# Optimization experiments

Hardware: AMD Instinct MI355X
Metric: run time of the kernel (lower is better)

Reference implementation:

```python
import jax, jax.numpy as jnp
import numpy as np

CH = 256
IC = 128  # inter_channels = channels // reduction
TEMP = 0.05


def setup_inputs() -> dict:
    key = jax.random.key(0)
    k1, k2, k3, k4, k5 = jax.random.split(key, 5)
    x = jax.random.normal(k1, (8, CH, 64, 64), dtype=jnp.float32)
    # 1x1 conv weights stored as [out_ch, in_ch]
    w_qkv = jax.random.normal(k2, (3 * IC, CH), dtype=jnp.float32) * 0.01
    b_qkv = jax.random.normal(k3, (3 * IC,), dtype=jnp.float32) * 0.01
    w_out = jax.random.normal(k4, (CH, IC), dtype=jnp.float32) * 0.01
    b_out = jax.random.normal(k5, (CH,), dtype=jnp.float32) * 0.01
    return {"x": x, "w_qkv": w_qkv, "b_qkv": b_qkv, "w_out": w_out, "b_out": b_out}


def reference(x, w_qkv, b_qkv, w_out, b_out):
    b, c, h, w = x.shape
    n = h * w
    ic = w_qkv.shape[0] // 3
    # 1x1 conv QKV projection
    qkv = jnp.einsum('bchw,oc->bohw', x, w_qkv) + b_qkv[None, :, None, None]
    qkv = qkv.reshape(b, 3, ic, n)
    q, k, v = qkv[:, 0], qkv[:, 1], qkv[:, 2]  # each [b, ic, n]
    # mean-center q and k over spatial positions (per channel)
    k = k - k.mean(axis=-1, keepdims=True)
    q = q - q.mean(axis=-1, keepdims=True)
    # pairwise_weight[b, i, j] = sum_c k[b, c, i] * q[b, c, j]
    pw = jnp.einsum('bci,bcj->bij', k, q)
    pw = pw / jnp.sqrt(jnp.float32(ic))  # use_scale=True
    pw = pw / TEMP
    pw = jax.nn.softmax(pw, axis=-1)  # [b, n, n]
    # y[b, c, i] = sum_j pw[b, i, j] * v[b, c, j]
    y = jnp.einsum('bij,bcj->bci', pw, v).reshape(b, ic, h, w)
    out = x + jnp.einsum('bchw,oc->bohw', y, w_out) + b_out[None, :, None, None]
    return out
```

## Files before the change

kernel.cpp:

```cpp
#include <hip/hip_runtime.h>
#include <hip/hip_bf16.h>

typedef __bf16 bf16_t;
typedef __bf16 bf16x8 __attribute__((ext_vector_type(8)));
typedef float f32x4 __attribute__((ext_vector_type(4)));
typedef float f32x16 __attribute__((ext_vector_type(16)));

#define MFMA16(a, b, c) __builtin_amdgcn_mfma_f32_16x16x32_bf16((a), (b), (c), 0, 0, 0)
#define MFMA32(a, b, c) __builtin_amdgcn_mfma_f32_32x32x16_bf16((a), (b), (c), 0, 0, 0)

constexpr int CH = 256, IC = 128, NPOS = 4096;
constexpr float SM_C = 2.5503488f;

constexpr size_t OFF_XT    = 0;
constexpr size_t OFF_QT    = 16777216;
constexpr size_t OFF_KT    = 25165824;
constexpr size_t OFF_V     = 33554432;
constexpr size_t OFF_WQKV  = 41943040;
constexpr size_t OFF_WOUT  = 42139648;
constexpr size_t OFF_QKM   = 42213376;
constexpr size_t OFF_PL    = 42221568;

__device__ __forceinline__ void gload_lds16(const char* g, char* lds) {
    __builtin_amdgcn_global_load_lds((const __attribute__((address_space(1))) unsigned int*)g,
                                     (__attribute__((address_space(3))) unsigned int*)lds, 16, 0,
                                     0);
}
__device__ __forceinline__ float fexp2(float x) {
    float r;
    asm("v_exp_f32 %0, %1" : "=v"(r) : "v"(x));
    return r;
}
__device__ __forceinline__ int cvtpk(float lo, float hi) {
    int r;
    asm("v_cvt_pk_bf16_f32 %0, %1, %2" : "=v"(r) : "v"(lo), "v"(hi));
    return r;
}

__global__ void k_prep1(const float* __restrict__ x, const float* __restrict__ wqkv,
                        const float* __restrict__ wout, bf16_t* __restrict__ xt,
                        float* __restrict__ xpart, bf16_t* __restrict__ wqkv_b,
                        bf16_t* __restrict__ wout_b) {
    int bid = blockIdx.x;
    if (bid >= 8192) {
        int idx = (bid - 8192) * 256 + threadIdx.x;
        if (idx < 384 * 256) wqkv_b[idx] = (bf16_t)wqkv[idx];
        int j = idx - 384 * 256;
        if (j >= 0 && j < 256 * 128) wout_b[j] = (bf16_t)wout[j];
        return;
    }
    __shared__ float t[32][33];
    int p0 = (bid & 127) * 32, c0 = ((bid >> 7) & 7) * 32, b = bid >> 10;
    int i = threadIdx.x >> 5, j = threadIdx.x & 31;
#pragma unroll
    for (int q = 0; q < 4; q++) {
        int c = c0 + q * 8 + i;
        t[q * 8 + i][j] = x[((size_t)(b * CH + c)) * NPOS + p0 + j];
    }
    __syncthreads();
#pragma unroll
    for (int q = 0; q < 4; q++) {
        int p = p0 + q * 8 + i;
        xt[((size_t)(b * NPOS + p)) * CH + c0 + j] = (bf16_t)t[j][q * 8 + i];
    }
    int cl = threadIdx.x >> 3, part = threadIdx.x & 7;
    float s = 0.f;
#pragma unroll
    for (int u = 0; u < 4; u++) s += t[cl][part * 4 + u];
    s += __shfl_down(s, 4, 64);
    s += __shfl_down(s, 2, 64);
    s += __shfl_down(s, 1, 64);
    if (part == 0) xpart[((size_t)(b * 128) + (p0 >> 5)) * 256 + c0 + cl] = s;
}

__global__ void k_small(const float* __restrict__ xpart, const float* __restrict__ wqkv,
                        float* __restrict__ qkm) {
    int b = blockIdx.x, t = threadIdx.x;
    __shared__ float xm[256];
    float s = 0.f;
    const float* xp = xpart + (size_t)(b * 128) * 256 + t;
#pragma unroll 8
    for (int i = 0; i < 128; i++) s += xp[i * 256];
    xm[t] = s * (1.0f / NPOS);
    __syncthreads();
    float acc = 0.f;
    const float4* w = (const float4*)(wqkv + (size_t)t * CH);
#pragma unroll
    for (int c4 = 0; c4 < 64; c4++) {
        float4 w4 = w[c4];
        acc += w4.x * xm[c4 * 4] + w4.y * xm[c4 * 4 + 1] + w4.z * xm[c4 * 4 + 2] +
               w4.w * xm[c4 * 4 + 3];
    }
    qkm[b * CH + t] = acc;
}

__global__ __launch_bounds__(256, 2) void k_qkv(const bf16_t* __restrict__ xt,
                                                const bf16_t* __restrict__ wqkv_b,
                                                const float* __restrict__ qkm,
                                                const float* __restrict__ b_qkv,
                                                bf16_t* __restrict__ qt, bf16_t* __restrict__ kt,
                                                bf16_t* __restrict__ v) {
    int bid = blockIdx.x;
    int b = bid & 7;
    int r0 = bid >> 3;
    int sec = r0 % 3;
    int pt = r0 / 3;
    int p0 = pt * 128;
    int wid = threadIdx.x >> 6, lane = threadIdx.x & 63;
    int g = lane >> 4, li = lane & 15;
    int wr = wid >> 1, wc = wid & 1;
    f32x4 acc[4][4] = {};
    if (sec < 2) {
        int ob = sec * 128;
#pragma unroll 1
        for (int kk = 0; kk < 8; kk++) {
            bf16x8 af[4], bfg[4];
#pragma unroll
            for (int fa = 0; fa < 4; fa++) {
                int p = p0 + wr * 64 + fa * 16 + li;
                af[fa] = *(const bf16x8*)(xt + ((size_t)(b * NPOS + p)) * CH + kk * 32 + g * 8);
            }
#pragma unroll
            for (int fb = 0; fb < 4; fb++) {
                int o = ob + wc * 64 + fb * 16 + li;
                bfg[fb] = *(const bf16x8*)(wqkv_b + (size_t)o * CH + kk * 32 + g * 8);
            }
#pragma unroll
            for (int fa = 0; fa < 4; fa++)
#pragma unroll
                for (int fb = 0; fb < 4; fb++) acc[fa][fb] = MFMA16(af[fa], bfg[fb], acc[fa][fb]);
        }
        bf16_t* dst = (sec == 0) ? qt : kt;
        float scale = (sec == 1) ? SM_C : 1.0f;
#pragma unroll
        for (int fb = 0; fb < 4; fb++) {
            int ol = wc * 64 + fb * 16 + li;
            float mean = qkm[b * CH + sec * 128 + ol];
#pragma unroll
            for (int fa = 0; fa < 4; fa++)
#pragma unroll
                for (int r = 0; r < 4; r++) {
                    int p = p0 + wr * 64 + fa * 16 + g * 4 + r;
                    dst[((size_t)(b * NPOS + p)) * IC + ol] =
                        (bf16_t)((acc[fa][fb][r] - mean) * scale);
                }
        }
    } else {
#pragma unroll 1
        for (int kk = 0; kk < 8; kk++) {
            bf16x8 af[4], bfg[4];
#pragma unroll
            for (int fa = 0; fa < 4; fa++) {
                int o = 256 + wr * 64 + fa * 16 + li;
                af[fa] = *(const bf16x8*)(wqkv_b + (size_t)o * CH + kk * 32 + g * 8);
            }
#pragma unroll
            for (int fb = 0; fb < 4; fb++) {
                int p = p0 + wc * 64 + fb * 16 + li;
                bfg[fb] = *(const bf16x8*)(xt + ((size_t)(b * NPOS + p)) * CH + kk * 32 + g * 8);
            }
#pragma unroll
            for (int fa = 0; fa < 4; fa++)
#pragma unroll
                for (int fb = 0; fb < 4; fb++) acc[fa][fb] = MFMA16(af[fa], bfg[fb], acc[fa][fb]);
        }
#pragma unroll
        for (int fa = 0; fa < 4; fa++)
#pragma unroll
            for (int r = 0; r < 4; r++) {
                int oe = wr * 64 + fa * 16 + g * 4 + r;
                float bias = b_qkv[256 + oe];
#pragma unroll
                for (int fb = 0; fb < 4; fb++) {
                    int p = p0 + wc * 64 + fb * 16 + li;
                    v[((size_t)(b * IC + oe)) * NPOS + p] = (bf16_t)(acc[fa][fb][r] + bias);
                }
            }
    }
}

constexpr int TJ = 32;

__global__ __launch_bounds__(256, 2) void k_attn(const bf16_t* __restrict__ qt,
                                                 const bf16_t* __restrict__ kt,
                                                 const bf16_t* __restrict__ v,
                                                 bf16_t* __restrict__ pacc,
                                                 float* __restrict__ pl) {
    __shared__ __attribute__((aligned(128))) char smem[2 * 16384];
    const int bid = blockIdx.x;
    const int b = bid & 7;
    const int jh = (bid >> 3) & 1;
    const int it = bid >> 4;
    const int jbase = jh * 2048;
    const int t = threadIdx.x;
    const int wid = t >> 6, lane = t & 63;
    const int col = lane & 31, h = lane >> 5;
    const int iw0 = it * 128 + wid * 32;
    const bf16_t* ktb = kt + (size_t)b * NPOS * IC;
    const bf16_t* qtb = qt + (size_t)b * NPOS * IC;
    const bf16_t* vb = v + (size_t)b * IC * NPOS;

    int qoff_[2], voff_[2];
#pragma unroll
    for (int u = 0; u < 2; u++) {
        int li2 = u * 256 + t;
        int row = li2 >> 4, p = li2 & 15;
        qoff_[u] = row * 256 + ((p ^ (row & 15)) << 4);
        int g = p ^ (row & 15);
        int c = (g >> 2) * 32 + row;
        voff_[u] = c * 8192 + (g & 3) * 16;
    }

    auto stage = [&](int dstpar, int sj) {
        const char* qs = (const char*)qtb + (size_t)sj * 256;
        const char* vs = (const char*)vb + (size_t)sj * 2;
        char* qd = smem + dstpar * 16384;
        char* vd = qd + 8192;
#pragma unroll
        for (int u = 0; u < 2; u++) {
            gload_lds16(qs + qoff_[u], qd + (u * 256 + t) * 16);
            gload_lds16(vs + voff_[u], vd + (u * 256 + t) * 16);
        }
    };

    bf16x8 bk[8];
#pragma unroll
    for (int ks = 0; ks < 8; ks++)
        bk[ks] = *(const bf16x8*)(ktb + (size_t)(iw0 + col) * IC + ks * 16 + h * 8);

    stage(0, jbase);

    f32x16 acc[4] = {};
    float ls[4] = {0.f, 0.f, 0.f, 0.f};

    auto body = [&](int par, int nextj) {
        stage(par ^ 1, nextj);
        asm volatile("s_waitcnt vmcnt(4)" ::: "memory");
        __builtin_amdgcn_s_barrier();
        asm volatile("" ::: "memory");
        const char* qb = smem + par * 16384;
        const char* vbuf = qb + 8192;
        f32x16 s = {};
        __builtin_amdgcn_s_setprio(1);
#pragma unroll
        for (int ks = 0; ks < 8; ks++) {
            bf16x8 aq = *(const bf16x8*)(qb + col * 256 + (((ks * 2 + h) ^ (col & 15)) << 4));
            s = MFMA32(aq, bk[ks], s);
        }
        __builtin_amdgcn_s_setprio(0);
        float e[16];
#pragma unroll
        for (int r = 0; r < 16; r++) e[r] = fexp2(s[r]);
#pragma unroll
        for (int r = 0; r < 16; r++) ls[r & 3] += e[r];
        int w[8];
#pragma unroll
        for (int q = 0; q < 8; q++) w[q] = cvtpk(e[2 * q], e[2 * q + 1]);
        asm("v_permlane32_swap_b32 %0, %1" : "+v"(w[0]), "+v"(w[2]));
        asm("v_permlane32_swap_b32 %0, %1" : "+v"(w[1]), "+v"(w[3]));
        asm("v_permlane32_swap_b32 %0, %1" : "+v"(w[4]), "+v"(w[6]));
        asm("v_permlane32_swap_b32 %0, %1" : "+v"(w[5]), "+v"(w[7]));
        union {
            int u[4];
            bf16x8 v;
        } pb0, pb1;
        pb0.u[0] = w[0]; pb0.u[1] = w[1]; pb0.u[2] = w[2]; pb0.u[3] = w[3];
        pb1.u[0] = w[4]; pb1.u[1] = w[5]; pb1.u[2] = w[6]; pb1.u[3] = w[7];
        __builtin_amdgcn_s_setprio(1);
#pragma unroll
        for (int kg = 0; kg < 2; kg++) {
            bf16x8 pbf = kg == 0 ? pb0.v : pb1.v;
#pragma unroll
            for (int cs = 0; cs < 4; cs++) {
                bf16x8 av = *(const bf16x8*)(vbuf + col * 256 +
                                             (((cs * 4 + kg * 2 + h) ^ (col & 15)) << 4));
                acc[cs] = MFMA32(av, pbf, acc[cs]);
            }
        }
        __builtin_amdgcn_s_setprio(0);
        asm volatile("" ::: "memory");
        __builtin_amdgcn_s_barrier();
    };

#pragma unroll 1
    for (int jo = 0; jo < 2048; jo += 2 * TJ) {
        body(0, jbase + ((jo + TJ) & 2047));
        body(1, jbase + ((jo + 2 * TJ) & 2047));
    }

    float lsum = (ls[0] + ls[1]) + (ls[2] + ls[3]);
    lsum += __shfl_xor(lsum, 32, 64);
    const int i = iw0 + col;
    if (h == 0) pl[((size_t)(b * 2 + jh)) * NPOS + i] = lsum;

    bf16_t* po = pacc + ((size_t)(b * 2 + jh)) * NPOS * IC;
#pragma unroll
    for (int cs = 0; cs < 4; cs++)
#pragma unroll
        for (int q = 0; q < 8; q++) {
            int u = cvtpk(acc[cs][2 * q], acc[cs][2 * q + 1]);
            int c0 = cs * 32 + ((q & 1) << 1) + ((q >> 1) << 3) + 4 * h;
            *(int*)((char*)po + ((size_t)i * IC + c0) * 2) = u;
        }
}

__global__ __launch_bounds__(256, 2) void k_out(const bf16_t* __restrict__ pacc,
                                                const float* __restrict__ pl,
                                                const bf16_t* __restrict__ wout_b,
                                                const float* __restrict__ x,
                                                const float* __restrict__ b_out,
                                                float* __restrict__ out) {
    int bid = blockIdx.x;
    int b = bid & 7;
    int r0 = bid >> 3;
    int oct = r0 & 1, pt = r0 >> 1;
    int p0 = pt * 128, oc0 = oct * 128;
    int wid = threadIdx.x >> 6, lane = threadIdx.x & 63;
    int g = lane >> 4, li = lane & 15;
    int wr = wid >> 1, wc = wid & 1;
    const bf16_t* pa0 = pacc + (size_t)(b * 2 + 0) * NPOS * IC;
    const bf16_t* pa1 = pacc + (size_t)(b * 2 + 1) * NPOS * IC;
    float inv[4];
#pragma unroll
    for (int fb = 0; fb < 4; fb++) {
        int p = p0 + wc * 64 + fb * 16 + li;
        inv[fb] = 1.0f / (pl[(size_t)(b * 2 + 0) * NPOS + p] + pl[(size_t)(b * 2 + 1) * NPOS + p]);
    }
    f32x4 acc[4][4] = {};
#pragma unroll
    for (int kk = 0; kk < 4; kk++) {
        bf16x8 af[4], bfg[4];
#pragma unroll
        for (int fa = 0; fa < 4; fa++) {
            int oc = oc0 + wr * 64 + fa * 16 + li;
            af[fa] = *(const bf16x8*)(wout_b + (size_t)oc * IC + kk * 32 + g * 8);
        }
#pragma unroll
        for (int fb = 0; fb < 4; fb++) {
            int p = p0 + wc * 64 + fb * 16 + li;
            bf16x8 a0 = *(const bf16x8*)(pa0 + (size_t)p * IC + kk * 32 + g * 8);
            bf16x8 a1 = *(const bf16x8*)(pa1 + (size_t)p * IC + kk * 32 + g * 8);
#pragma unroll
            for (int e = 0; e < 8; e++)
                bfg[fb][e] = (bf16_t)(((float)a0[e] + (float)a1[e]) * inv[fb]);
        }
#pragma unroll
        for (int fa = 0; fa < 4; fa++)
#pragma unroll
            for (int fb = 0; fb < 4; fb++) acc[fa][fb] = MFMA16(af[fa], bfg[fb], acc[fa][fb]);
    }
#pragma unroll
    for (int fa = 0; fa < 4; fa++)
#pragma unroll
        for (int r = 0; r < 4; r++) {
            int oc = oc0 + wr * 64 + fa * 16 + g * 4 + r;
            float bias = b_out[oc];
#pragma unroll
            for (int fb = 0; fb < 4; fb++) {
                int p = p0 + wc * 64 + fb * 16 + li;
                size_t idx = ((size_t)(b * CH + oc)) * NPOS + p;
                out[idx] = acc[fa][fb][r] + x[idx] + bias;
            }
        }
}

extern "C" void kernel_launch(void* const* d_in, const int* in_sizes, int n_in, void* d_out,
                              int out_size, void* d_ws, size_t ws_size, hipStream_t stream) {
    const float* x = (const float*)d_in[0];
    const float* w_qkv = (const float*)d_in[1];
    const float* b_qkv = (const float*)d_in[2];
    const float* w_out = (const float*)d_in[3];
    const float* b_out = (const float*)d_in[4];
    float* out = (float*)d_out;
    char* ws = (char*)d_ws;

    bf16_t* xt = (bf16_t*)(ws + OFF_XT);
    bf16_t* pacc = (bf16_t*)(ws + OFF_XT);
    bf16_t* qt = (bf16_t*)(ws + OFF_QT);
    bf16_t* kt = (bf16_t*)(ws + OFF_KT);
    bf16_t* v = (bf16_t*)(ws + OFF_V);
    float* xpart = (float*)(ws + OFF_V);
    bf16_t* wqkv_b = (bf16_t*)(ws + OFF_WQKV);
    bf16_t* wout_b = (bf16_t*)(ws + OFF_WOUT);
    float* qkm = (float*)(ws + OFF_QKM);
    float* pl = (float*)(ws + OFF_PL);

    k_prep1<<<8704, 256, 0, stream>>>(x, w_qkv, w_out, xt, xpart, wqkv_b, wout_b);
    k_small<<<8, 256, 0, stream>>>(xpart, w_qkv, qkm);
    k_qkv<<<768, 256, 0, stream>>>(xt, wqkv_b, qkm, b_qkv, qt, kt, v);
    k_attn<<<512, 256, 0, stream>>>(qt, kt, v, pacc, pl);
    k_out<<<512, 256, 0, stream>>>(pacc, pl, wout_b, x, b_out, out);
}
```

Baseline: 152.4 us.

## Load Q tiles directly into registers instead of staging through LDS

The attention kernel now loads each wave's Q fragment straight from global memory into registers, prefetching the next tile after the score MFMAs, and only stages V through LDS. This halves the shared memory footprint and removes the LDS reads for Q. The cost is that every wave fetches the same Q rows separately from global memory or L2, and the extra registers held for the prefetched fragments may raise register pressure. The vmcnt wait threshold is adjusted to match, but it does not account for the outstanding direct Q loads, so the ordering of the wait may be off.

```diff
diff --git a/kernel.cpp b/kernel.cpp
--- a/kernel.cpp
+++ b/kernel.cpp
@@ -186,7 +186,7 @@
                                                  const bf16_t* __restrict__ v,
                                                  bf16_t* __restrict__ pacc,
                                                  float* __restrict__ pl) {
-    __shared__ __attribute__((aligned(128))) char smem[2 * 16384];
+    __shared__ __attribute__((aligned(128))) char smem[2 * 8192];
     const int bid = blockIdx.x;
     const int b = bid & 7;
     const int jh = (bid >> 3) & 1;
@@ -200,54 +200,53 @@
     const bf16_t* qtb = qt + (size_t)b * NPOS * IC;
     const bf16_t* vb = v + (size_t)b * IC * NPOS;
 
-    int qoff_[2], voff_[2];
+    int voff_[2];
 #pragma unroll
     for (int u = 0; u < 2; u++) {
         int li2 = u * 256 + t;
         int row = li2 >> 4, p = li2 & 15;
-        qoff_[u] = row * 256 + ((p ^ (row & 15)) << 4);
         int g = p ^ (row & 15);
         int c = (g >> 2) * 32 + row;
         voff_[u] = c * 8192 + (g & 3) * 16;
     }
 
-    auto stage = [&](int dstpar, int sj) {
-        const char* qs = (const char*)qtb + (size_t)sj * 256;
+    auto stageV = [&](int dstpar, int sj) {
         const char* vs = (const char*)vb + (size_t)sj * 2;
-        char* qd = smem + dstpar * 16384;
-        char* vd = qd + 8192;
-#pragma unroll
-        for (int u = 0; u < 2; u++) {
-            gload_lds16(qs + qoff_[u], qd + (u * 256 + t) * 16);
-            gload_lds16(vs + voff_[u], vd + (u * 256 + t) * 16);
-        }
+        char* vd = smem + dstpar * 8192;
+#pragma unroll
+        for (int u = 0; u < 2; u++) gload_lds16(vs + voff_[u], vd + (u * 256 + t) * 16);
     };
+
+    const char* qrow = (const char*)qtb + col * 256 + h * 16;
 
     bf16x8 bk[8];
 #pragma unroll
     for (int ks = 0; ks < 8; ks++)
         bk[ks] = *(const bf16x8*)(ktb + (size_t)(iw0 + col) * IC + ks * 16 + h * 8);
 
-    stage(0, jbase);
+    stageV(0, jbase);
+    bf16x8 aq[8];
+#pragma unroll
+    for (int ks = 0; ks < 8; ks++)
+        aq[ks] = *(const bf16x8*)(qrow + (size_t)jbase * 256 + ks * 32);
 
     f32x16 acc[4] = {};
     float ls[4] = {0.f, 0.f, 0.f, 0.f};
 
     auto body = [&](int par, int nextj) {
-        stage(par ^ 1, nextj);
-        asm volatile("s_waitcnt vmcnt(4)" ::: "memory");
+        stageV(par ^ 1, nextj);
+        asm volatile("s_waitcnt vmcnt(2)" ::: "memory");
         __builtin_amdgcn_s_barrier();
         asm volatile("" ::: "memory");
-        const char* qb = smem + par * 16384;
-        const char* vbuf = qb + 8192;
+        const char* vbuf = smem + par * 8192;
         f32x16 s = {};
         __builtin_amdgcn_s_setprio(1);
 #pragma unroll
-        for (int ks = 0; ks < 8; ks++) {
-            bf16x8 aq = *(const bf16x8*)(qb + col * 256 + (((ks * 2 + h) ^ (col & 15)) << 4));
-            s = MFMA32(aq, bk[ks], s);
-        }
+        for (int ks = 0; ks < 8; ks++) s = MFMA32(aq[ks], bk[ks], s);
         __builtin_amdgcn_s_setprio(0);
+#pragma unroll
+        for (int ks = 0; ks < 8; ks++)
+            aq[ks] = *(const bf16x8*)(qrow + (size_t)nextj * 256 + ks * 32);
         float e[16];
 #pragma unroll
         for (int r = 0; r < 16; r++) e[r] = fexp2(s[r]);
```

Measured after the change: 219.3 us. 1.44x slower.
